# Performance work log

Hardware: AMD Instinct MI355X
Metric: run time of the kernel (lower is better)

The kernel has to match this reference:

```python
import jax, jax.numpy as jnp
import numpy as np
import math

D_MODEL = 2048
Q_HEAD = 32
KV_HEAD = 8
HEAD_DIM = D_MODEL // Q_HEAD  # 64
GROUP = Q_HEAD // KV_HEAD     # 4
B, T = 2, 2048


def setup_inputs() -> dict:
    key = jax.random.key(0)
    ks = jax.random.split(key, 9)
    s = 0.02
    return {
        "x": jax.random.normal(ks[0], (B, T, D_MODEL), dtype=jnp.float32),
        "Wq": jax.random.normal(ks[1], (D_MODEL, Q_HEAD * HEAD_DIM), dtype=jnp.float32) * s,
        "bq": jnp.zeros((Q_HEAD * HEAD_DIM,), dtype=jnp.float32),
        "Wk": jax.random.normal(ks[2], (D_MODEL, KV_HEAD * HEAD_DIM), dtype=jnp.float32) * s,
        "bk": jnp.zeros((KV_HEAD * HEAD_DIM,), dtype=jnp.float32),
        "Wv": jax.random.normal(ks[3], (D_MODEL, KV_HEAD * HEAD_DIM), dtype=jnp.float32) * s,
        "bv": jnp.zeros((KV_HEAD * HEAD_DIM,), dtype=jnp.float32),
        "Wo": jax.random.normal(ks[4], (D_MODEL, D_MODEL), dtype=jnp.float32) * s,
        "bo": jnp.zeros((D_MODEL,), dtype=jnp.float32),
    }


def reference(x, Wq, bq, Wk, bk, Wv, bv, Wo, bo):
    Bx, Tx, C = x.shape
    # projections -> [B, H, T, Dh]
    q = (x @ Wq + bq).reshape(Bx, Tx, Q_HEAD, HEAD_DIM).transpose(0, 2, 1, 3)
    k = (x @ Wk + bk).reshape(Bx, Tx, KV_HEAD, HEAD_DIM).transpose(0, 2, 1, 3)
    v = (x @ Wv + bv).reshape(Bx, Tx, KV_HEAD, HEAD_DIM).transpose(0, 2, 1, 3)
    # GQA: repeat each KV head `GROUP` times (repeat_interleave semantics)
    k = jnp.repeat(k, GROUP, axis=1)
    v = jnp.repeat(v, GROUP, axis=1)
    score = jnp.einsum("bhqd,bhkd->bhqk", q, k) / math.sqrt(HEAD_DIM)
    causal = jnp.tril(jnp.ones((Tx, Tx), dtype=bool))
    score = jnp.where(causal, score, -jnp.inf)
    attn = jax.nn.softmax(score, axis=-1)
    out = jnp.einsum("bhqk,bhkd->bhqd", attn, v)
    out = out.transpose(0, 2, 1, 3).reshape(Bx, Tx, C)
    return out @ Wo + bo
```

## Files before the change

kernel.cpp:

```cpp
#include <hip/hip_runtime.h>
#include <hip/hip_bf16.h>

typedef unsigned short u16;
typedef __attribute__((ext_vector_type(8)))  __bf16 bf16x8;
typedef __attribute__((ext_vector_type(8)))  unsigned short u16x8;
typedef __attribute__((ext_vector_type(4)))  unsigned short u16x4;
typedef __attribute__((ext_vector_type(4)))  float f32x4;

#define MFMA(a, b, c) __builtin_amdgcn_mfma_f32_16x16x32_bf16((a), (b), (c), 0, 0, 0)

__device__ __forceinline__ u16 f2b(float f) {
  union { float f; unsigned u; } x; x.f = f;
  unsigned r = x.u + 0x7fffu + ((x.u >> 16) & 1u);
  return (u16)(r >> 16);
}

__device__ __forceinline__ void gl_lds16(void* lds, const void* g) {
  __builtin_amdgcn_global_load_lds(
      (const __attribute__((address_space(1))) void*)g,
      (__attribute__((address_space(3))) void*)lds, 16, 0, 0);
}

__global__ __launch_bounds__(256) void cvt_kernel(const float* __restrict__ in,
                                                  u16* __restrict__ out, int n) {
  int i = (blockIdx.x * 256 + threadIdx.x) * 4;
  if (i >= n) return;
  f32x4 v = *(const f32x4*)(in + i);
  u16x4 o;
  o[0] = f2b(v[0]); o[1] = f2b(v[1]); o[2] = f2b(v[2]); o[3] = f2b(v[3]);
  *(u16x4*)(out + i) = o;
}

__global__ __launch_bounds__(256) void cvt_t_kernel(const float* __restrict__ W,
                                                    u16* __restrict__ Wt, int K, int N) {
  __shared__ u16 t[32][33];
  const int n0 = blockIdx.x * 32, k0 = blockIdx.y * 32;
  const int tc = threadIdx.x & 31, tr = threadIdx.x >> 5;
#pragma unroll
  for (int i = 0; i < 4; i++)
    t[tr + i * 8][tc] = f2b(W[(size_t)(k0 + tr + i * 8) * N + n0 + tc]);
  __syncthreads();
#pragma unroll
  for (int i = 0; i < 4; i++)
    Wt[(size_t)(n0 + tr + i * 8) * K + k0 + tc] = t[tc][tr + i * 8];
}

template <bool OUT_BF16>
__device__ __forceinline__ void gemm_body(const u16* __restrict__ A, const u16* __restrict__ Bt,
                                          const float* __restrict__ bias, void* __restrict__ C,
                                          const int N, const int n0, const int m0, const float scale) {
  __shared__ __align__(16) u16 As[128 * 32];
  __shared__ __align__(16) u16 Bs[128 * 32];
  const int lane = threadIdx.x & 63, wv = threadIdx.x >> 6;
  const int l15 = lane & 15, lg = lane >> 4;
  const int wm = wv >> 1, wn = wv & 1;
  const int rowQ = lane >> 2;
  const int g = lane & 3;

  f32x4 acc[4][4] = {};

  for (int k0 = 0; k0 < 2048; k0 += 32) {
#pragma unroll
    for (int c = 0; c < 2; c++) {
      const int cc = c * 4 + wv;
      const int row = cc * 16 + rowQ;
      const int gs = g ^ ((row >> 1) & 3);
      gl_lds16(&As[cc * 512], A + (((size_t)(m0 + row)) << 11) + k0 + gs * 8);
      gl_lds16(&Bs[cc * 512], Bt + (((size_t)(n0 + row)) << 11) + k0 + gs * 8);
    }
    __syncthreads();
    bf16x8 af[4], bfr[4];
#pragma unroll
    for (int t = 0; t < 4; t++) {
      const int ra = wm * 64 + t * 16 + l15;
      af[t] = *(const bf16x8*)&As[ra * 32 + ((lg ^ ((ra >> 1) & 3)) << 3)];
      const int rb = wn * 64 + t * 16 + l15;
      bfr[t] = *(const bf16x8*)&Bs[rb * 32 + ((lg ^ ((rb >> 1) & 3)) << 3)];
    }
#pragma unroll
    for (int mt = 0; mt < 4; mt++)
#pragma unroll
      for (int nt = 0; nt < 4; nt++)
        acc[mt][nt] = MFMA(af[mt], bfr[nt], acc[mt][nt]);
    __syncthreads();
  }

#pragma unroll
  for (int nt = 0; nt < 4; nt++) {
    const int col = n0 + wn * 64 + nt * 16 + l15;
    const float bc = bias[col];
#pragma unroll
    for (int mt = 0; mt < 4; mt++) {
#pragma unroll
      for (int r = 0; r < 4; r++) {
        const int row = m0 + wm * 64 + mt * 16 + lg * 4 + r;
        const float v = (acc[mt][nt][r] + bc) * scale;
        if (OUT_BF16) ((u16*)C)[(size_t)row * N + col] = f2b(v);
        else          ((float*)C)[(size_t)row * N + col] = v;
      }
    }
  }
}

__global__ __launch_bounds__(256) void qkv_gemm_kernel(
    const u16* __restrict__ xb,
    const u16* __restrict__ Wqt, const u16* __restrict__ Wkt, const u16* __restrict__ Wvt,
    const float* __restrict__ bq, const float* __restrict__ bk, const float* __restrict__ bv,
    u16* __restrict__ Qb, u16* __restrict__ Kb, u16* __restrict__ Vb) {
  const int nb = blockIdx.x;
  const u16* Bt; const float* bias; u16* out; int N, n0; float scale;
  if (nb < 16)      { Bt = Wqt; bias = bq; out = Qb; N = 2048; n0 = nb * 128;        scale = 0.125f * 1.44269504f; }
  else if (nb < 20) { Bt = Wkt; bias = bk; out = Kb; N = 512;  n0 = (nb - 16) * 128; scale = 1.0f; }
  else              { Bt = Wvt; bias = bv; out = Vb; N = 512;  n0 = (nb - 20) * 128; scale = 1.0f; }
  gemm_body<true>(xb, Bt, bias, out, N, n0, blockIdx.y * 128, scale);
}

__global__ __launch_bounds__(256) void oproj_kernel(const u16* __restrict__ Ab,
                                                    const u16* __restrict__ Wot,
                                                    const float* __restrict__ bo,
                                                    float* __restrict__ out) {
  gemm_body<false>(Ab, Wot, bo, out, 2048, blockIdx.x * 128, blockIdx.y * 128, 1.0f);
}

__global__ __launch_bounds__(1024) void attn_kernel(const u16* __restrict__ Qb,
                                                    const u16* __restrict__ Kb,
                                                    const u16* __restrict__ Vb,
                                                    u16* __restrict__ Ab) {
  const int pr = blockIdx.x, kh = blockIdx.y, b = blockIdx.z;
  const int tid = threadIdx.x;
  const int lane = tid & 63, wv = tid >> 6;
  const int hh = wv & 3, qq = wv >> 2;
  const int h = kh * 4 + hh;
  const int l15 = lane & 15, lg = lane >> 4;

  __shared__ __align__(16) u16 Ks[2][64 * 64];
  __shared__ __align__(16) u16 Vt[2][64 * 64];
  __shared__ __align__(16) u16 Ps[16][16 * 72];

  const int skv = (tid & 511) >> 3;
  const int sc8 = tid & 7;
  const int sd0 = sc8 * 8;
  const bool kRole = (wv < 8);

  const u16* Kbase = Kb + (size_t)(b * 2048) * 512 + kh * 64;
  const u16* Vbase = Vb + (size_t)(b * 2048) * 512 + kh * 64;
  u16* Pw = Ps[wv];

  __bf16 one1 = (__bf16)1.0f;
  bf16x8 ones = {one1, one1, one1, one1, one1, one1, one1, one1};

  for (int sel = 0; sel < 2; sel++) {
    const int qt = sel ? 31 - pr : pr;
    const int q0 = qt * 64;

    bf16x8 qf[2];
    {
      const u16* qp = Qb + (size_t)(b * 2048 + q0 + qq * 16 + l15) * 2048 + h * 64 + lg * 8;
      qf[0] = *(const bf16x8*)(qp);
      qf[1] = *(const bf16x8*)(qp + 32);
    }
    f32x4 o[4] = {};
    f32x4 os = {};
    float mrow[4] = {-1e30f, -1e30f, -1e30f, -1e30f};

    __syncthreads();
    int cur = 0;
    if (kRole) {
      gl_lds16(&Ks[0][wv * 512], Kbase + ((size_t)skv << 9) + ((sc8 ^ (skv & 7)) << 3));
    } else {
      u16x8 vr = *(const u16x8*)(Vbase + ((size_t)skv << 9) + sd0);
#pragma unroll
      for (int j = 0; j < 8; j++) {
        const int jj = (j + sc8) & 7;
        const int d = sd0 + jj;
        Vt[0][d * 64 + (skv ^ ((d & 7) << 3))] = vr[jj];
      }
    }
    for (int it = 0; it <= qt; ++it) {
      __syncthreads();
      const bool pre = (it < qt);
      u16x8 vnx;
      if (pre) {
        const size_t roff = (size_t)((it + 1) * 64 + skv) << 9;
        if (kRole) gl_lds16(&Ks[cur ^ 1][wv * 512], Kbase + roff + ((sc8 ^ (skv & 7)) << 3));
        else       vnx = *(const u16x8*)(Vbase + roff + sd0);
      }
      f32x4 sc[4] = {};
#pragma unroll
      for (int kt = 0; kt < 4; kt++) {
        const int krow = kt * 16 + l15;
#pragma unroll
        for (int ks = 0; ks < 2; ks++) {
          bf16x8 kf = *(const bf16x8*)&Ks[cur][krow * 64 + ((ks * 32 + lg * 8) ^ ((krow & 7) << 3))];
          sc[kt] = MFMA(qf[ks], kf, sc[kt]);
        }
      }
      if (it == qt) {
#pragma unroll
        for (int kt = 0; kt < 4; kt++)
#pragma unroll
          for (int r = 0; r < 4; r++) {
            const int q = qq * 16 + lg * 4 + r;
            const int kv = kt * 16 + l15;
            if (kv > q) sc[kt][r] = -1e30f;
          }
      }
      float tmax[4];
#pragma unroll
      for (int r = 0; r < 4; r++)
        tmax[r] = fmaxf(fmaxf(sc[0][r], sc[1][r]), fmaxf(sc[2][r], sc[3][r]));
#pragma unroll
      for (int m = 1; m < 16; m <<= 1)
#pragma unroll
        for (int r = 0; r < 4; r++)
          tmax[r] = fmaxf(tmax[r], __shfl_xor(tmax[r], m));
      int need = 0;
#pragma unroll
      for (int r = 0; r < 4; r++) need |= (tmax[r] > mrow[r] + 8.0f) ? 1 : 0;
      if (__any(need)) {
#pragma unroll
        for (int r = 0; r < 4; r++) {
          const float mnew = fmaxf(mrow[r], tmax[r]);
          const float scl = __builtin_amdgcn_exp2f(mrow[r] - mnew);
          mrow[r] = mnew;
          os[r] *= scl;
#pragma unroll
          for (int dt = 0; dt < 4; dt++) o[dt][r] *= scl;
        }
      }
#pragma unroll
      for (int kt = 0; kt < 4; kt++)
#pragma unroll
        for (int r = 0; r < 4; r++) {
          const float pv = __builtin_amdgcn_exp2f(sc[kt][r] - mrow[r]);
          const __bf16 pb = (__bf16)pv;
          Pw[(lg * 4 + r) * 72 + kt * 16 + l15] = __builtin_bit_cast(u16, pb);
        }
#pragma unroll
      for (int ks = 0; ks < 2; ks++) {
        bf16x8 pf = *(const bf16x8*)&Pw[l15 * 72 + ks * 32 + lg * 8];
        os = MFMA(pf, ones, os);
#pragma unroll
        for (int dt = 0; dt < 4; dt++) {
          const int drow = dt * 16 + l15;
          bf16x8 vf = *(const bf16x8*)&Vt[cur][drow * 64 + ((ks * 32 + lg * 8) ^ ((drow & 7) << 3))];
          o[dt] = MFMA(pf, vf, o[dt]);
        }
      }
      if (pre && !kRole) {
#pragma unroll
        for (int j = 0; j < 8; j++) {
          const int jj = (j + sc8) & 7;
          const int d = sd0 + jj;
          Vt[cur ^ 1][d * 64 + (skv ^ ((d & 7) << 3))] = vnx[jj];
        }
      }
      cur ^= 1;
    }
    float inv[4];
#pragma unroll
    for (int r = 0; r < 4; r++) inv[r] = 1.0f / os[r];
#pragma unroll
    for (int dt = 0; dt < 4; dt++)
#pragma unroll
      for (int r = 0; r < 4; r++) {
        const int q = q0 + qq * 16 + lg * 4 + r;
        Ab[(size_t)(b * 2048 + q) * 2048 + h * 64 + dt * 16 + l15] = f2b(o[dt][r] * inv[r]);
      }
  }
}

extern "C" void kernel_launch(void* const* d_in, const int* in_sizes, int n_in,
                              void* d_out, int out_size, void* d_ws, size_t ws_size,
                              hipStream_t stream) {
  const float* x  = (const float*)d_in[0];
  const float* Wq = (const float*)d_in[1];
  const float* bq = (const float*)d_in[2];
  const float* Wk = (const float*)d_in[3];
  const float* bk = (const float*)d_in[4];
  const float* Wv = (const float*)d_in[5];
  const float* bv = (const float*)d_in[6];
  const float* Wo = (const float*)d_in[7];
  const float* bo = (const float*)d_in[8];

  char* ws = (char*)d_ws;
  u16* xb  = (u16*)(ws + 0);
  u16* Ab  = (u16*)(ws + 0);
  u16* Qb  = (u16*)(ws + 16777216);
  u16* Kb  = (u16*)(ws + 33554432);
  u16* Vb  = (u16*)(ws + 37748736);
  u16* Wqt = (u16*)(ws + 41943040);
  u16* Wkt = (u16*)(ws + 50331648);
  u16* Wvt = (u16*)(ws + 52428800);
  u16* Wot = (u16*)(ws + 54525952);

  cvt_kernel<<<8192, 256, 0, stream>>>(x, xb, 2 * 2048 * 2048);
  cvt_t_kernel<<<dim3(64, 64), 256, 0, stream>>>(Wq, Wqt, 2048, 2048);
  cvt_t_kernel<<<dim3(16, 64), 256, 0, stream>>>(Wk, Wkt, 2048, 512);
  cvt_t_kernel<<<dim3(16, 64), 256, 0, stream>>>(Wv, Wvt, 2048, 512);
  cvt_t_kernel<<<dim3(64, 64), 256, 0, stream>>>(Wo, Wot, 2048, 2048);

  qkv_gemm_kernel<<<dim3(24, 32), 256, 0, stream>>>(xb, Wqt, Wkt, Wvt, bq, bk, bv, Qb, Kb, Vb);
  attn_kernel<<<dim3(16, 8, 2), 1024, 0, stream>>>(Qb, Kb, Vb, Ab);
  oproj_kernel<<<dim3(16, 32), 256, 0, stream>>>(Ab, Wot, bo, (float*)d_out);
}
```

Before: 248.1 us.

## Rewrite attention kernel with 32x32 MFMA tiles and 512-thread blocks

```diff
diff --git a/kernel.cpp b/kernel.cpp
--- a/kernel.cpp
+++ b/kernel.cpp
@@ -6,13 +6,20 @@
 typedef __attribute__((ext_vector_type(8)))  unsigned short u16x8;
 typedef __attribute__((ext_vector_type(4)))  unsigned short u16x4;
 typedef __attribute__((ext_vector_type(4)))  float f32x4;
-
-#define MFMA(a, b, c) __builtin_amdgcn_mfma_f32_16x16x32_bf16((a), (b), (c), 0, 0, 0)
+typedef __attribute__((ext_vector_type(16))) float f32x16;
+
+#define MFMA(a, b, c)   __builtin_amdgcn_mfma_f32_16x16x32_bf16((a), (b), (c), 0, 0, 0)
+#define MFMA32(a, b, c) __builtin_amdgcn_mfma_f32_32x32x16_bf16((a), (b), (c), 0, 0, 0)
 
 __device__ __forceinline__ u16 f2b(float f) {
   union { float f; unsigned u; } x; x.f = f;
   unsigned r = x.u + 0x7fffu + ((x.u >> 16) & 1u);
   return (u16)(r >> 16);
+}
+
+__device__ __forceinline__ unsigned pack2(float lo, float hi) {
+  const __bf16 a = (__bf16)lo, b = (__bf16)hi;
+  return (unsigned)__builtin_bit_cast(u16, a) | ((unsigned)__builtin_bit_cast(u16, b) << 16);
 }
 
 __device__ __forceinline__ void gl_lds16(void* lds, const void* g) {
@@ -122,58 +129,52 @@
   gemm_body<false>(Ab, Wot, bo, out, 2048, blockIdx.x * 128, blockIdx.y * 128, 1.0f);
 }
 
-__global__ __launch_bounds__(1024) void attn_kernel(const u16* __restrict__ Qb,
-                                                    const u16* __restrict__ Kb,
-                                                    const u16* __restrict__ Vb,
-                                                    u16* __restrict__ Ab) {
+__global__ __launch_bounds__(512, 4) void attn_kernel(const u16* __restrict__ Qb,
+                                                      const u16* __restrict__ Kb,
+                                                      const u16* __restrict__ Vb,
+                                                      u16* __restrict__ Ab) {
   const int pr = blockIdx.x, kh = blockIdx.y, b = blockIdx.z;
   const int tid = threadIdx.x;
   const int lane = tid & 63, wv = tid >> 6;
-  const int hh = wv & 3, qq = wv >> 2;
+  const int hh = wv & 3, qh = wv >> 2;
   const int h = kh * 4 + hh;
-  const int l15 = lane & 15, lg = lane >> 4;
-
-  __shared__ __align__(16) u16 Ks[2][64 * 64];
-  __shared__ __align__(16) u16 Vt[2][64 * 64];
-  __shared__ __align__(16) u16 Ps[16][16 * 72];
-
-  const int skv = (tid & 511) >> 3;
+  const int l31 = lane & 31, hi = lane >> 5;
+  const int swz = (l31 & 7) << 3;
+
+  __shared__ __align__(16) u16 lds[16384];
+  __shared__ __align__(16) u16 Ps[8][32 * 72];
+
+  const int skv = tid >> 3;
   const int sc8 = tid & 7;
   const int sd0 = sc8 * 8;
-  const bool kRole = (wv < 8);
 
   const u16* Kbase = Kb + (size_t)(b * 2048) * 512 + kh * 64;
   const u16* Vbase = Vb + (size_t)(b * 2048) * 512 + kh * 64;
   u16* Pw = Ps[wv];
 
-  __bf16 one1 = (__bf16)1.0f;
-  bf16x8 ones = {one1, one1, one1, one1, one1, one1, one1, one1};
-
   for (int sel = 0; sel < 2; sel++) {
     const int qt = sel ? 31 - pr : pr;
     const int q0 = qt * 64;
 
-    bf16x8 qf[2];
+    bf16x8 qf[4];
     {
-      const u16* qp = Qb + (size_t)(b * 2048 + q0 + qq * 16 + l15) * 2048 + h * 64 + lg * 8;
-      qf[0] = *(const bf16x8*)(qp);
-      qf[1] = *(const bf16x8*)(qp + 32);
-    }
-    f32x4 o[4] = {};
-    f32x4 os = {};
-    float mrow[4] = {-1e30f, -1e30f, -1e30f, -1e30f};
+      const u16* qp = Qb + (size_t)(b * 2048 + q0 + qh * 32 + l31) * 2048 + h * 64 + hi * 8;
+#pragma unroll
+      for (int c = 0; c < 4; c++) qf[c] = *(const bf16x8*)(qp + c * 16);
+    }
+    f32x16 ot[2] = {};
+    float mrow = -30000.0f, srow = 0.f;
 
     __syncthreads();
     int cur = 0;
-    if (kRole) {
-      gl_lds16(&Ks[0][wv * 512], Kbase + ((size_t)skv << 9) + ((sc8 ^ (skv & 7)) << 3));
-    } else {
+    {
+      gl_lds16(lds + (wv << 9), Kbase + ((size_t)skv << 9) + ((sc8 ^ (skv & 7)) << 3));
       u16x8 vr = *(const u16x8*)(Vbase + ((size_t)skv << 9) + sd0);
 #pragma unroll
       for (int j = 0; j < 8; j++) {
         const int jj = (j + sc8) & 7;
         const int d = sd0 + jj;
-        Vt[0][d * 64 + (skv ^ ((d & 7) << 3))] = vr[jj];
+        lds[8192 + d * 64 + (skv ^ ((d & 7) << 3))] = vr[jj];
       }
     }
     for (int it = 0; it <= qt; ++it) {
@@ -182,91 +183,99 @@
       u16x8 vnx;
       if (pre) {
         const size_t roff = (size_t)((it + 1) * 64 + skv) << 9;
-        if (kRole) gl_lds16(&Ks[cur ^ 1][wv * 512], Kbase + roff + ((sc8 ^ (skv & 7)) << 3));
-        else       vnx = *(const u16x8*)(Vbase + roff + sd0);
-      }
-      f32x4 sc[4] = {};
-#pragma unroll
-      for (int kt = 0; kt < 4; kt++) {
-        const int krow = kt * 16 + l15;
-#pragma unroll
-        for (int ks = 0; ks < 2; ks++) {
-          bf16x8 kf = *(const bf16x8*)&Ks[cur][krow * 64 + ((ks * 32 + lg * 8) ^ ((krow & 7) << 3))];
-          sc[kt] = MFMA(qf[ks], kf, sc[kt]);
+        gl_lds16(lds + ((cur ^ 1) << 12) + (wv << 9), Kbase + roff + ((sc8 ^ (skv & 7)) << 3));
+        vnx = *(const u16x8*)(Vbase + roff + sd0);
+      }
+      const u16* Kc = lds + (cur << 12);
+      const u16* Vc = lds + 8192 + (cur << 12);
+
+      f32x16 sc2[2] = {};
+#pragma unroll
+      for (int c = 0; c < 4; c++) {
+        const int dblk = (c * 16 + hi * 8) ^ swz;
+#pragma unroll
+        for (int kvh = 0; kvh < 2; kvh++) {
+          bf16x8 kf = *(const bf16x8*)&Kc[(kvh * 32 + l31) * 64 + dblk];
+          sc2[kvh] = MFMA32(kf, qf[c], sc2[kvh]);
         }
       }
       if (it == qt) {
-#pragma unroll
-        for (int kt = 0; kt < 4; kt++)
-#pragma unroll
-          for (int r = 0; r < 4; r++) {
-            const int q = qq * 16 + lg * 4 + r;
-            const int kv = kt * 16 + l15;
-            if (kv > q) sc[kt][r] = -1e30f;
+        const int q = qh * 32 + l31;
+#pragma unroll
+        for (int kvh = 0; kvh < 2; kvh++)
+#pragma unroll
+          for (int r = 0; r < 16; r++) {
+            const int kv = kvh * 32 + (r & 3) + 8 * (r >> 2) + 4 * hi;
+            if (kv > q) sc2[kvh][r] = -30000.0f;
           }
       }
-      float tmax[4];
-#pragma unroll
-      for (int r = 0; r < 4; r++)
-        tmax[r] = fmaxf(fmaxf(sc[0][r], sc[1][r]), fmaxf(sc[2][r], sc[3][r]));
-#pragma unroll
-      for (int m = 1; m < 16; m <<= 1)
-#pragma unroll
-        for (int r = 0; r < 4; r++)
-          tmax[r] = fmaxf(tmax[r], __shfl_xor(tmax[r], m));
-      int need = 0;
-#pragma unroll
-      for (int r = 0; r < 4; r++) need |= (tmax[r] > mrow[r] + 8.0f) ? 1 : 0;
-      if (__any(need)) {
-#pragma unroll
-        for (int r = 0; r < 4; r++) {
-          const float mnew = fmaxf(mrow[r], tmax[r]);
-          const float scl = __builtin_amdgcn_exp2f(mrow[r] - mnew);
-          mrow[r] = mnew;
-          os[r] *= scl;
-#pragma unroll
-          for (int dt = 0; dt < 4; dt++) o[dt][r] *= scl;
+      float tm = fmaxf(sc2[0][0], sc2[0][1]);
+#pragma unroll
+      for (int kvh = 0; kvh < 2; kvh++)
+#pragma unroll
+        for (int r = (kvh ? 0 : 2); r < 16; r++) tm = fmaxf(tm, sc2[kvh][r]);
+      tm = fmaxf(tm, __shfl_xor(tm, 32));
+      if (__any(tm > mrow + 8.0f)) {
+        const float mnew = fmaxf(mrow, tm);
+        const float scl = __builtin_amdgcn_exp2f(mrow - mnew);
+        mrow = mnew;
+        srow *= scl;
+#pragma unroll
+        for (int dh = 0; dh < 2; dh++)
+#pragma unroll
+          for (int r = 0; r < 16; r++) ot[dh][r] *= scl;
+      }
+      float ps = 0.f;
+#pragma unroll
+      for (int kvh = 0; kvh < 2; kvh++)
+#pragma unroll
+        for (int j = 0; j < 8; j++) {
+          const float p0 = __builtin_amdgcn_exp2f(sc2[kvh][2 * j] - mrow);
+          const float p1 = __builtin_amdgcn_exp2f(sc2[kvh][2 * j + 1] - mrow);
+          ps += p0 + p1;
+          const int kvB = kvh * 32 + 8 * (j >> 1) + 2 * (j & 1) + 4 * hi;
+          *(unsigned*)&Pw[l31 * 72 + kvB] = pack2(p0, p1);
         }
-      }
-#pragma unroll
-      for (int kt = 0; kt < 4; kt++)
-#pragma unroll
-        for (int r = 0; r < 4; r++) {
-          const float pv = __builtin_amdgcn_exp2f(sc[kt][r] - mrow[r]);
-          const __bf16 pb = (__bf16)pv;
-          Pw[(lg * 4 + r) * 72 + kt * 16 + l15] = __builtin_bit_cast(u16, pb);
+      ps += __shfl_xor(ps, 32);
+      srow += ps;
+#pragma unroll
+      for (int t = 0; t < 4; t++) {
+        const bf16x8 pf = *(const bf16x8*)&Pw[l31 * 72 + t * 16 + hi * 8];
+        const int kblk = ((t * 16 + hi * 8) ^ swz);
+#pragma unroll
+        for (int dh = 0; dh < 2; dh++) {
+          bf16x8 vf = *(const bf16x8*)&Vc[(dh * 32 + l31) * 64 + kblk];
+          ot[dh] = MFMA32(vf, pf, ot[dh]);
         }
-#pragma unroll
-      for (int ks = 0; ks < 2; ks++) {
-        bf16x8 pf = *(const bf16x8*)&Pw[l15 * 72 + ks * 32 + lg * 8];
-        os = MFMA(pf, ones, os);
-#pragma unroll
-        for (int dt = 0; dt < 4; dt++) {
-          const int drow = dt * 16 + l15;
-          bf16x8 vf = *(const bf16x8*)&Vt[cur][drow * 64 + ((ks * 32 + lg * 8) ^ ((drow & 7) << 3))];
-          o[dt] = MFMA(pf, vf, o[dt]);
-        }
-      }
-      if (pre && !kRole) {
+      }
+      if (pre) {
 #pragma unroll
         for (int j = 0; j < 8; j++) {
           const int jj = (j + sc8) & 7;
           const int d = sd0 + jj;
-          Vt[cur ^ 1][d * 64 + (skv ^ ((d & 7) << 3))] = vnx[jj];
+          lds[8192 + ((cur ^ 1) << 12) + d * 64 + (skv ^ ((d & 7) << 3))] = vnx[jj];
         }
       }
       cur ^= 1;
     }
-    float inv[4];
-#pragma unroll
-    for (int r = 0; r < 4; r++) inv[r] = 1.0f / os[r];
-#pragma unroll
-    for (int dt = 0; dt < 4; dt++)
-#pragma unroll
-      for (int r = 0; r < 4; r++) {
-        const int q = q0 + qq * 16 + lg * 4 + r;
-        Ab[(size_t)(b * 2048 + q) * 2048 + h * 64 + dt * 16 + l15] = f2b(o[dt][r] * inv[r]);
-      }
+    __syncthreads();
+    u16* Sx = lds + wv * 2048;
+    const float inv = 1.0f / srow;
+#pragma unroll
+    for (int dh = 0; dh < 2; dh++)
+#pragma unroll
+      for (int jr = 0; jr < 8; jr++) {
+        const unsigned w = pack2(ot[dh][2 * jr] * inv, ot[dh][2 * jr + 1] * inv);
+        const int d = dh * 32 + 8 * (jr >> 1) + (jr & 1) * 2 + 4 * hi;
+        *(unsigned*)&Sx[l31 * 64 + (d ^ swz)] = w;
+      }
+#pragma unroll
+    for (int rep = 0; rep < 4; rep++) {
+      const int chunk = rep * 64 + lane;
+      const int qr = chunk >> 3, cc = chunk & 7;
+      u16x8 val = *(const u16x8*)&Sx[qr * 64 + ((cc * 8) ^ ((qr & 7) << 3))];
+      *(u16x8*)&Ab[(size_t)(b * 2048 + q0 + qh * 32 + qr) * 2048 + h * 64 + cc * 8] = val;
+    }
   }
 }
 
@@ -301,6 +310,6 @@
   cvt_t_kernel<<<dim3(64, 64), 256, 0, stream>>>(Wo, Wot, 2048, 2048);
 
   qkv_gemm_kernel<<<dim3(24, 32), 256, 0, stream>>>(xb, Wqt, Wkt, Wvt, bq, bk, bv, Qb, Kb, Vb);
-  attn_kernel<<<dim3(16, 8, 2), 1024, 0, stream>>>(Qb, Kb, Vb, Ab);
+  attn_kernel<<<dim3(16, 8, 2), 512, 0, stream>>>(Qb, Kb, Vb, Ab);
   oproj_kernel<<<dim3(16, 32), 256, 0, stream>>>(Ab, Wot, bo, (float*)d_out);
 }
```

Result: slower. 259.0 us (+4.4%).
